# Kernel optimization log

Measured on AMD Instinct MI355X. Metric: run time of the kernel, lower is better.

## Reference

```python
import jax, jax.numpy as jnp
import numpy as np

IN, H, OUT, B = 1024, 4096, 1, 4096


def setup_inputs() -> dict:
    key = jax.random.key(0)
    ks = jax.random.split(key, 20)
    sx = 1.0 / np.sqrt(IN)
    sh = 1.0 / np.sqrt(H)
    d = {
        "x": jax.random.normal(ks[0], (B, IN), jnp.float32),
        "hidden": jax.random.normal(ks[1], (B, H), jnp.float32),
        "cell": jax.random.normal(ks[2], (B, H), jnp.float32),
        # input projections (Linear(input_size, h_size)), weight [H, IN], bias [H]
        "Wx_i": jax.random.normal(ks[3], (H, IN), jnp.float32) * sx,
        "Wx_f": jax.random.normal(ks[4], (H, IN), jnp.float32) * sx,
        "Wx_o": jax.random.normal(ks[5], (H, IN), jnp.float32) * sx,
        "Wx_c": jax.random.normal(ks[6], (H, IN), jnp.float32) * sx,
        "bx_i": jax.random.normal(ks[7], (H,), jnp.float32) * sx,
        "bx_f": jax.random.normal(ks[8], (H,), jnp.float32) * sx,
        "bx_o": jax.random.normal(ks[9], (H,), jnp.float32) * sx,
        "bx_c": jax.random.normal(ks[10], (H,), jnp.float32) * sx,
        # hidden projections (Linear(h_size, h_size, bias=False)), weight [H, H]
        "Wh_i": jax.random.normal(ks[11], (H, H), jnp.float32) * sh,
        "Wh_f": jax.random.normal(ks[12], (H, H), jnp.float32) * sh,
        "Wh_o": jax.random.normal(ks[13], (H, H), jnp.float32) * sh,
        "Wh_c": jax.random.normal(ks[14], (H, H), jnp.float32) * sh,
        # output head Linear(h_size, out_size)
        "Wy": jax.random.normal(ks[15], (OUT, H), jnp.float32) * sh,
        "by": jax.random.normal(ks[16], (OUT,), jnp.float32) * sh,
    }
    return d


def reference(x, hidden, cell,
              Wx_i, Wx_f, Wx_o, Wx_c,
              bx_i, bx_f, bx_o, bx_c,
              Wh_i, Wh_f, Wh_o, Wh_c,
              Wy, by):
    # single LSTM step, batched over leading dim
    i = jax.nn.sigmoid(x @ Wx_i.T + bx_i + hidden @ Wh_i.T)
    f = jax.nn.sigmoid(x @ Wx_f.T + bx_f + hidden @ Wh_f.T)
    o = jax.nn.sigmoid(x @ Wx_o.T + bx_o + hidden @ Wh_o.T)
    c_til = jnp.tanh(x @ Wx_c.T + bx_c + hidden @ Wh_c.T)
    c_new = f * cell + i * c_til
    h_new = o * jnp.tanh(c_new)
    y_hat = h_new @ Wy.T + by  # [B, OUT]
    return y_hat
```

## Files before the change

kernel.cpp:

```cpp
#include <hip/hip_runtime.h>
#include <stdint.h>

#define IN_ 1024
#define H_  4096
#define B_  4096
#define K_  5120
#define NT_ 80

typedef short bf16x8 __attribute__((ext_vector_type(8)));
typedef float f32x4  __attribute__((ext_vector_type(4)));

__device__ __forceinline__ unsigned short f2bf(float x) {
    union { float f; uint32_t u; } v; v.f = x;
    return (unsigned short)((v.u + 0x7FFFu + ((v.u >> 16) & 1u)) >> 16);
}
__device__ __forceinline__ float bf2f(uint32_t u16) {
    union { uint32_t u; float f; } v; v.u = u16 << 16; return v.f;
}

__global__ __launch_bounds__(256) void cvt_cat(
    const float* __restrict__ s1, const float* __restrict__ s2,
    unsigned short* __restrict__ dst)
{
    int idx = blockIdx.x * 256 + threadIdx.x;
    int r = idx / (K_ / 4);
    int c = (idx % (K_ / 4)) * 4;
    float4 v;
    if (c < IN_) v = *(const float4*)(s1 + (size_t)r * IN_ + c);
    else         v = *(const float4*)(s2 + (size_t)r * H_ + (c - IN_));
    ushort4 o = { f2bf(v.x), f2bf(v.y), f2bf(v.z), f2bf(v.w) };
    *(ushort4*)(dst + (size_t)r * K_ + c) = o;
}

__device__ __forceinline__ int swz(int row) { return ((row >> 1) & 3) << 4; }

__global__ __launch_bounds__(512, 2) void gemm_gate8(
    const unsigned short* __restrict__ A,
    const unsigned short* __restrict__ W,
    const float* __restrict__ bias,
    unsigned short* __restrict__ P)
{
    __shared__ __align__(16) char ldsb[131072];

    const int tid  = threadIdx.x;
    const int wid  = tid >> 6;
    const int lane = tid & 63;

    const int wg = (blockIdx.x & 7) * 32 + (blockIdx.x >> 3);
    const int mt = wg & 15, nt = wg >> 4;
    const int bm = mt * 256, bn = nt * 256;

    const int wm = wid >> 2;
    const int wn = wid & 3;

    const int l15 = lane & 15;
    const int c0  = (lane >> 4) << 4;

    const int q0  = wid * 64 + lane;
    const int r0  = q0 >> 2;
    const int cb0 = ((q0 & 3) << 4) ^ swz(r0);
    const int r1  = r0 + 128;
    const int cb1 = ((q0 & 3) << 4) ^ swz(r1);

    f32x4 acc[8][4];
#pragma unroll
    for (int i = 0; i < 8; ++i)
#pragma unroll
        for (int j = 0; j < 4; ++j) acc[i][j] = (f32x4){0.f, 0.f, 0.f, 0.f};

    auto stage = [&](int isB, int ksel, int tau) {
        if (tau >= NT_) tau = NT_ - 2 + (tau & 1);
        const int kbase = tau * 64 + ksel * 32;
        const int chunk = (tau & 1) * 65536 + isB * 32768 + ksel * 16384;
        const unsigned short* src = isB ? W : A;
        const int gb = isB ? bn : bm;
        __builtin_amdgcn_global_load_lds(
            (const __attribute__((address_space(1))) void*)(src + (size_t)(gb + r0) * K_ + kbase + (cb0 >> 1)),
            (__attribute__((address_space(3))) void*)(ldsb + chunk + wid * 1024), 16, 0, 0);
        __builtin_amdgcn_global_load_lds(
            (const __attribute__((address_space(1))) void*)(src + (size_t)(gb + r1) * K_ + kbase + (cb1 >> 1)),
            (__attribute__((address_space(3))) void*)(ldsb + chunk + 8192 + wid * 1024), 16, 0, 0);
    };

    stage(0, 0, 0); stage(0, 1, 0); stage(1, 0, 0); stage(1, 1, 0);
    stage(1, 0, 1); stage(1, 1, 1);
    asm volatile("s_waitcnt vmcnt(4)" ::: "memory");
    __builtin_amdgcn_s_barrier();

    for (int i = 0; i < NT_ / 2; ++i) {
        const int T0 = 2 * i;
#pragma unroll
        for (int half = 0; half < 2; ++half) {
            const char* base  = ldsb + half * 65536;
            const char* Abase = base;
            const char* Bbase = base + 32768;

            bf16x8 b[2][4];
#pragma unroll
            for (int q = 0; q < 4; ++q) {
                bf16x8 a[2][2];
#pragma unroll
                for (int kh = 0; kh < 2; ++kh)
#pragma unroll
                    for (int mi = 0; mi < 2; ++mi) {
                        const int row = wm * 128 + q * 32 + mi * 16 + l15;
                        a[kh][mi] = *(const bf16x8*)(Abase + kh * 16384 + row * 64 + (c0 ^ swz(row)));
                    }
                if (q == 0) {
#pragma unroll
                    for (int kh = 0; kh < 2; ++kh)
#pragma unroll
                        for (int ni = 0; ni < 4; ++ni) {
                            const int row = wn * 64 + ni * 16 + l15;
                            b[kh][ni] = *(const bf16x8*)(Bbase + kh * 16384 + row * 64 + (c0 ^ swz(row)));
                        }
                }

                if (half == 0) {
                    if      (q == 0) stage(0, 0, T0 + 1);
                    else if (q == 1) stage(0, 1, T0 + 1);
                    else if (q == 2) stage(1, 0, T0 + 2);
                    else             stage(1, 1, T0 + 2);
                } else {
                    if      (q == 0) stage(0, 0, T0 + 2);
                    else if (q == 1) stage(0, 1, T0 + 2);
                    else if (q == 2) stage(1, 0, T0 + 3);
                    else             stage(1, 1, T0 + 3);
                }

                if (q == 0) asm volatile("s_waitcnt lgkmcnt(8)" ::: "memory");
                if (q == 3) asm volatile("s_waitcnt vmcnt(4)" ::: "memory");
                __builtin_amdgcn_s_barrier();
                asm volatile("s_waitcnt lgkmcnt(0)" ::: "memory");
                __builtin_amdgcn_sched_barrier(0);
                __builtin_amdgcn_s_setprio(1);
#pragma unroll
                for (int kh = 0; kh < 2; ++kh)
#pragma unroll
                    for (int mi = 0; mi < 2; ++mi)
#pragma unroll
                        for (int ni = 0; ni < 4; ++ni)
                            acc[q * 2 + mi][ni] = __builtin_amdgcn_mfma_f32_16x16x32_bf16(
                                a[kh][mi], b[kh][ni], acc[q * 2 + mi][ni], 0, 0, 0);
                __builtin_amdgcn_s_setprio(0);
                __builtin_amdgcn_s_barrier();
            }
        }
    }

#pragma unroll
    for (int ni = 0; ni < 4; ++ni) {
        const int col = bn + wn * 64 + ni * 16 + l15;
        const float bv = bias[col];
#pragma unroll
        for (int mi = 0; mi < 8; ++mi) {
            const int row0 = bm + wm * 128 + mi * 16 + (lane >> 4) * 4;
#pragma unroll
            for (int r = 0; r < 4; ++r)
                P[(size_t)(row0 + r) * H_ + col] = f2bf(acc[mi][ni][r] + bv);
        }
    }
}

__global__ __launch_bounds__(256) void gates_gemv(
    const unsigned short* __restrict__ Pi, const unsigned short* __restrict__ Pf,
    const unsigned short* __restrict__ Po, const unsigned short* __restrict__ Pc,
    const float* __restrict__ cell, const float* __restrict__ Wy,
    const float* __restrict__ by, float* __restrict__ y)
{
    const int b = blockIdx.x;
    const int t = threadIdx.x;
    const size_t base = (size_t)b * H_;
    float part = 0.f;

#pragma unroll
    for (int j = 0; j < 4; ++j) {
        const int h = j * 1024 + t * 4;
        const uint2 ri = *(const uint2*)(Pi + base + h);
        const uint2 rf = *(const uint2*)(Pf + base + h);
        const uint2 ro = *(const uint2*)(Po + base + h);
        const uint2 rc = *(const uint2*)(Pc + base + h);
        const float4 cv = *(const float4*)(cell + base + h);
        const float4 wv = *(const float4*)(Wy + h);

        const uint32_t zi[4] = { ri.x & 0xffffu, ri.x >> 16, ri.y & 0xffffu, ri.y >> 16 };
        const uint32_t zf[4] = { rf.x & 0xffffu, rf.x >> 16, rf.y & 0xffffu, rf.y >> 16 };
        const uint32_t zo[4] = { ro.x & 0xffffu, ro.x >> 16, ro.y & 0xffffu, ro.y >> 16 };
        const uint32_t zc[4] = { rc.x & 0xffffu, rc.x >> 16, rc.y & 0xffffu, rc.y >> 16 };
        const float cc[4] = { cv.x, cv.y, cv.z, cv.w };
        const float ww[4] = { wv.x, wv.y, wv.z, wv.w };
#pragma unroll
        for (int e = 0; e < 4; ++e) {
            const float ig = 1.f / (1.f + __expf(-bf2f(zi[e])));
            const float fg = 1.f / (1.f + __expf(-bf2f(zf[e])));
            const float og = 1.f / (1.f + __expf(-bf2f(zo[e])));
            const float ct = tanhf(bf2f(zc[e]));
            const float cn = fg * cc[e] + ig * ct;
            const float hn = og * tanhf(cn);
            part += hn * ww[e];
        }
    }

#pragma unroll
    for (int off = 32; off > 0; off >>= 1) part += __shfl_down(part, off, 64);
    __shared__ float red[4];
    if ((t & 63) == 0) red[t >> 6] = part;
    __syncthreads();
    if (t == 0) y[b] = red[0] + red[1] + red[2] + red[3] + by[0];
}

extern "C" void kernel_launch(void* const* d_in, const int* in_sizes, int n_in,
                              void* d_out, int out_size, void* d_ws, size_t ws_size,
                              hipStream_t stream) {
    const float* x      = (const float*)d_in[0];
    const float* hidden = (const float*)d_in[1];
    const float* cell   = (const float*)d_in[2];
    const float* Wx[4]  = { (const float*)d_in[3], (const float*)d_in[4],
                            (const float*)d_in[5], (const float*)d_in[6] };
    const float* bx[4]  = { (const float*)d_in[7], (const float*)d_in[8],
                            (const float*)d_in[9], (const float*)d_in[10] };
    const float* Wh[4]  = { (const float*)d_in[11], (const float*)d_in[12],
                            (const float*)d_in[13], (const float*)d_in[14] };
    const float* Wy     = (const float*)d_in[15];
    const float* by     = (const float*)d_in[16];
    float* y = (float*)d_out;

    unsigned short* Ab = (unsigned short*)d_ws;
    unsigned short* Wb = Ab + (size_t)B_ * K_;
    unsigned short* Pg[4];
    {
        unsigned short* p0 = Wb + (size_t)H_ * K_;
        for (int g = 0; g < 4; ++g) Pg[g] = p0 + (size_t)g * B_ * H_;
    }

    const int cvt_grid = (B_ * (K_ / 4)) / 256;
    cvt_cat<<<cvt_grid, 256, 0, stream>>>(x, hidden, Ab);

    for (int g = 0; g < 4; ++g) {
        cvt_cat<<<cvt_grid, 256, 0, stream>>>(Wx[g], Wh[g], Wb);
        gemm_gate8<<<256, 512, 0, stream>>>(Ab, Wb, bx[g], Pg[g]);
    }

    gates_gemv<<<B_, 256, 0, stream>>>(Pg[0], Pg[1], Pg[2], Pg[3], cell, Wy, by, y);
}
```

Measured before the change: 741.8 us.

## Restructure GEMM main loop to one barrier per substep and split-K MFMA issue

Flattens the half/q loops into one 8-step loop. Each step now has a single workgroup barrier instead of two, and the LDS fragment loads are reordered so the first K-half MFMAs can start before the second-half reads land. Global-to-LDS staging is issued after the barrier, and the vmcnt wait is loosened from 4 to 2. The aim is less barrier and LDS-wait stall and better overlap of LDS reads with MFMA. Dropping the trailing barrier risks a write-after-read race on the LDS buffers if the staging order no longer protects them.

After: 705.5 us. 1.05x faster.

```diff
diff --git a/kernel.cpp b/kernel.cpp
--- a/kernel.cpp
+++ b/kernel.cpp
@@ -89,62 +89,67 @@
 
     for (int i = 0; i < NT_ / 2; ++i) {
         const int T0 = 2 * i;
-#pragma unroll
-        for (int half = 0; half < 2; ++half) {
-            const char* base  = ldsb + half * 65536;
-            const char* Abase = base;
-            const char* Bbase = base + 32768;
-
-            bf16x8 b[2][4];
-#pragma unroll
-            for (int q = 0; q < 4; ++q) {
-                bf16x8 a[2][2];
-#pragma unroll
-                for (int kh = 0; kh < 2; ++kh)
-#pragma unroll
-                    for (int mi = 0; mi < 2; ++mi) {
-                        const int row = wm * 128 + q * 32 + mi * 16 + l15;
-                        a[kh][mi] = *(const bf16x8*)(Abase + kh * 16384 + row * 64 + (c0 ^ swz(row)));
-                    }
-                if (q == 0) {
-#pragma unroll
-                    for (int kh = 0; kh < 2; ++kh)
-#pragma unroll
-                        for (int ni = 0; ni < 4; ++ni) {
-                            const int row = wn * 64 + ni * 16 + l15;
-                            b[kh][ni] = *(const bf16x8*)(Bbase + kh * 16384 + row * 64 + (c0 ^ swz(row)));
-                        }
+        bf16x8 b[2][4];
+#pragma unroll
+        for (int k = 0; k < 8; ++k) {
+            const int half = k >> 2;
+            const int q    = k & 3;
+            const char* Abase = ldsb + half * 65536;
+            const char* Bbase = Abase + 32768;
+
+            bf16x8 a0[2], a1[2];
+            if (q == 0) {
+#pragma unroll
+                for (int ni = 0; ni < 4; ++ni) {
+                    const int row = wn * 64 + ni * 16 + l15;
+                    b[0][ni] = *(const bf16x8*)(Bbase + row * 64 + (c0 ^ swz(row)));
                 }
-
-                if (half == 0) {
-                    if      (q == 0) stage(0, 0, T0 + 1);
-                    else if (q == 1) stage(0, 1, T0 + 1);
-                    else if (q == 2) stage(1, 0, T0 + 2);
-                    else             stage(1, 1, T0 + 2);
-                } else {
-                    if      (q == 0) stage(0, 0, T0 + 2);
-                    else if (q == 1) stage(0, 1, T0 + 2);
-                    else if (q == 2) stage(1, 0, T0 + 3);
-                    else             stage(1, 1, T0 + 3);
+            }
+#pragma unroll
+            for (int mi = 0; mi < 2; ++mi) {
+                const int row = wm * 128 + q * 32 + mi * 16 + l15;
+                a0[mi] = *(const bf16x8*)(Abase + row * 64 + (c0 ^ swz(row)));
+            }
+            if (q == 0) {
+#pragma unroll
+                for (int ni = 0; ni < 4; ++ni) {
+                    const int row = wn * 64 + ni * 16 + l15;
+                    b[1][ni] = *(const bf16x8*)(Bbase + 16384 + row * 64 + (c0 ^ swz(row)));
                 }
-
-                if (q == 0) asm volatile("s_waitcnt lgkmcnt(8)" ::: "memory");
-                if (q == 3) asm volatile("s_waitcnt vmcnt(4)" ::: "memory");
-                __builtin_amdgcn_s_barrier();
-                asm volatile("s_waitcnt lgkmcnt(0)" ::: "memory");
-                __builtin_amdgcn_sched_barrier(0);
-                __builtin_amdgcn_s_setprio(1);
-#pragma unroll
-                for (int kh = 0; kh < 2; ++kh)
-#pragma unroll
-                    for (int mi = 0; mi < 2; ++mi)
-#pragma unroll
-                        for (int ni = 0; ni < 4; ++ni)
-                            acc[q * 2 + mi][ni] = __builtin_amdgcn_mfma_f32_16x16x32_bf16(
-                                a[kh][mi], b[kh][ni], acc[q * 2 + mi][ni], 0, 0, 0);
-                __builtin_amdgcn_s_setprio(0);
-                __builtin_amdgcn_s_barrier();
-            }
+            }
+#pragma unroll
+            for (int mi = 0; mi < 2; ++mi) {
+                const int row = wm * 128 + q * 32 + mi * 16 + l15;
+                a1[mi] = *(const bf16x8*)(Abase + 16384 + row * 64 + (c0 ^ swz(row)));
+            }
+
+            if (q == 3) asm volatile("s_waitcnt vmcnt(2)" ::: "memory");
+            __builtin_amdgcn_s_barrier();
+
+            if      (k == 0) stage(0, 0, T0 + 1);
+            else if (k == 1) stage(0, 1, T0 + 1);
+            else if (k == 2) stage(1, 0, T0 + 2);
+            else if (k == 3) stage(1, 1, T0 + 2);
+            else if (k == 4) stage(0, 0, T0 + 2);
+            else if (k == 5) stage(0, 1, T0 + 2);
+            else if (k == 6) stage(1, 0, T0 + 3);
+            else             stage(1, 1, T0 + 3);
+            __builtin_amdgcn_sched_barrier(0);
+
+            __builtin_amdgcn_s_setprio(1);
+#pragma unroll
+            for (int mi = 0; mi < 2; ++mi)
+#pragma unroll
+                for (int ni = 0; ni < 4; ++ni)
+                    acc[q * 2 + mi][ni] = __builtin_amdgcn_mfma_f32_16x16x32_bf16(
+                        a0[mi], b[0][ni], acc[q * 2 + mi][ni], 0, 0, 0);
+#pragma unroll
+            for (int mi = 0; mi < 2; ++mi)
+#pragma unroll
+                for (int ni = 0; ni < 4; ++ni)
+                    acc[q * 2 + mi][ni] = __builtin_amdgcn_mfma_f32_16x16x32_bf16(
+                        a1[mi], b[1][ni], acc[q * 2 + mi][ni], 0, 0, 0);
+            __builtin_amdgcn_s_setprio(0);
         }
     }
 
```

## Software-pipeline A-fragment LDS reads and reorder global-to-LDS staging in GEMM

Applied to the files above, without the earlier changes.

Restructures the main GEMM loop into an 8-step schedule that double-buffers A fragments in registers. The next step's A reads from LDS are issued before the current step's MFMAs, so LDS latency overlaps compute. Staging of the next tiles into LDS now happens after the MFMAs rather than before the barrier. The prologue now stages both buffers fully, and one barrier per step replaces two. The change raises register pressure and carries a risk of LDS read/write races, because stage writes now follow reads with fewer barriers.

Result: faster. 714.2 us, median of 4 (-3.7%).

```diff
diff --git a/kernel.cpp b/kernel.cpp
--- a/kernel.cpp
+++ b/kernel.cpp
@@ -82,69 +82,73 @@
             (__attribute__((address_space(3))) void*)(ldsb + chunk + 8192 + wid * 1024), 16, 0, 0);
     };
 
+    auto read_a = [&](bf16x8 dst[2][2], int kn) {
+        const char* Ab = ldsb + (kn >> 2) * 65536;
+        const int  nq  = kn & 3;
+#pragma unroll
+        for (int kh = 0; kh < 2; ++kh)
+#pragma unroll
+            for (int mi = 0; mi < 2; ++mi) {
+                const int row = wm * 128 + nq * 32 + mi * 16 + l15;
+                dst[kh][mi] = *(const bf16x8*)(Ab + kh * 16384 + row * 64 + (c0 ^ swz(row)));
+            }
+    };
+
     stage(0, 0, 0); stage(0, 1, 0); stage(1, 0, 0); stage(1, 1, 0);
-    stage(1, 0, 1); stage(1, 1, 1);
-    asm volatile("s_waitcnt vmcnt(4)" ::: "memory");
+    stage(0, 0, 1); stage(0, 1, 1); stage(1, 0, 1); stage(1, 1, 1);
+    asm volatile("s_waitcnt vmcnt(8)" ::: "memory");
     __builtin_amdgcn_s_barrier();
+
+    bf16x8 afrag[2][2][2];
+    bf16x8 b[2][4];
+    read_a(afrag[0], 0);
 
     for (int i = 0; i < NT_ / 2; ++i) {
         const int T0 = 2 * i;
 #pragma unroll
-        for (int half = 0; half < 2; ++half) {
-            const char* base  = ldsb + half * 65536;
-            const char* Abase = base;
-            const char* Bbase = base + 32768;
-
-            bf16x8 b[2][4];
-#pragma unroll
-            for (int q = 0; q < 4; ++q) {
-                bf16x8 a[2][2];
+        for (int k = 0; k < 8; ++k) {
+            const int q   = k & 3;
+            const int par = k & 1;
+            const char* Bbase = ldsb + (k >> 2) * 65536 + 32768;
+
+            if (q == 0) {
 #pragma unroll
                 for (int kh = 0; kh < 2; ++kh)
 #pragma unroll
-                    for (int mi = 0; mi < 2; ++mi) {
-                        const int row = wm * 128 + q * 32 + mi * 16 + l15;
-                        a[kh][mi] = *(const bf16x8*)(Abase + kh * 16384 + row * 64 + (c0 ^ swz(row)));
+                    for (int ni = 0; ni < 4; ++ni) {
+                        const int row = wn * 64 + ni * 16 + l15;
+                        b[kh][ni] = *(const bf16x8*)(Bbase + kh * 16384 + row * 64 + (c0 ^ swz(row)));
                     }
-                if (q == 0) {
-#pragma unroll
-                    for (int kh = 0; kh < 2; ++kh)
-#pragma unroll
-                        for (int ni = 0; ni < 4; ++ni) {
-                            const int row = wn * 64 + ni * 16 + l15;
-                            b[kh][ni] = *(const bf16x8*)(Bbase + kh * 16384 + row * 64 + (c0 ^ swz(row)));
-                        }
-                }
-
-                if (half == 0) {
-                    if      (q == 0) stage(0, 0, T0 + 1);
-                    else if (q == 1) stage(0, 1, T0 + 1);
-                    else if (q == 2) stage(1, 0, T0 + 2);
-                    else             stage(1, 1, T0 + 2);
-                } else {
-                    if      (q == 0) stage(0, 0, T0 + 2);
-                    else if (q == 1) stage(0, 1, T0 + 2);
-                    else if (q == 2) stage(1, 0, T0 + 3);
-                    else             stage(1, 1, T0 + 3);
-                }
-
-                if (q == 0) asm volatile("s_waitcnt lgkmcnt(8)" ::: "memory");
-                if (q == 3) asm volatile("s_waitcnt vmcnt(4)" ::: "memory");
-                __builtin_amdgcn_s_barrier();
-                asm volatile("s_waitcnt lgkmcnt(0)" ::: "memory");
-                __builtin_amdgcn_sched_barrier(0);
-                __builtin_amdgcn_s_setprio(1);
-#pragma unroll
-                for (int kh = 0; kh < 2; ++kh)
-#pragma unroll
-                    for (int mi = 0; mi < 2; ++mi)
-#pragma unroll
-                        for (int ni = 0; ni < 4; ++ni)
-                            acc[q * 2 + mi][ni] = __builtin_amdgcn_mfma_f32_16x16x32_bf16(
-                                a[kh][mi], b[kh][ni], acc[q * 2 + mi][ni], 0, 0, 0);
-                __builtin_amdgcn_s_setprio(0);
-                __builtin_amdgcn_s_barrier();
             }
+            if (q == 3) asm volatile("s_waitcnt vmcnt(4)" ::: "memory");
+            __builtin_amdgcn_s_barrier();
+
+            read_a(afrag[par ^ 1], (k + 1) & 7);
+            __builtin_amdgcn_sched_barrier(0);
+
+            __builtin_amdgcn_s_setprio(1);
+#pragma unroll
+            for (int mi = 0; mi < 2; ++mi)
+#pragma unroll
+                for (int ni = 0; ni < 4; ++ni)
+                    acc[q * 2 + mi][ni] = __builtin_amdgcn_mfma_f32_16x16x32_bf16(
+                        afrag[par][0][mi], b[0][ni], acc[q * 2 + mi][ni], 0, 0, 0);
+#pragma unroll
+            for (int mi = 0; mi < 2; ++mi)
+#pragma unroll
+                for (int ni = 0; ni < 4; ++ni)
+                    acc[q * 2 + mi][ni] = __builtin_amdgcn_mfma_f32_16x16x32_bf16(
+                        afrag[par][1][mi], b[1][ni], acc[q * 2 + mi][ni], 0, 0, 0);
+            __builtin_amdgcn_s_setprio(0);
+
+            if      (k == 0) stage(1, 0, T0 + 2);
+            else if (k == 1) stage(1, 1, T0 + 2);
+            else if (k == 2) stage(0, 0, T0 + 2);
+            else if (k == 3) stage(0, 1, T0 + 2);
+            else if (k == 4) stage(1, 0, T0 + 3);
+            else if (k == 5) stage(1, 1, T0 + 3);
+            else if (k == 6) stage(0, 0, T0 + 3);
+            else             stage(0, 1, T0 + 3);
         }
     }
 
```
